# Performance work log

Measured on AMD Instinct MI355X. Metric: run time of the kernel, lower is better.

Reference implementation:

```python
import jax, jax.numpy as jnp
import numpy as np

D_K = 64
NEG_INF = -1.0e9


def setup_inputs() -> dict:
    key = jax.random.key(0)
    kq, kk, kv, km = jax.random.split(key, 4)
    B, H, S, D = 4, 16, 2048, D_K
    q = jax.random.normal(kq, (B, H, S, D), dtype=jnp.float32)
    k = jax.random.normal(kk, (B, H, S, D), dtype=jnp.float32)
    v = jax.random.normal(kv, (B, H, S, D), dtype=jnp.float32)
    attn_mask = jax.random.randint(km, (B, H, S, S), 0, 2).astype(jnp.bool_)
    return {"q": q, "k": k, "v": v, "attn_mask": attn_mask}


def reference(q, k, v, attn_mask):
    # scores: [B,H,S,S] = q @ k^T / sqrt(d_k)
    scale = 1.0 / jnp.sqrt(jnp.float32(D_K)).astype(q.dtype)
    attn_score = jnp.einsum("bhqd,bhkd->bhqk", q, k) * scale
    attn_score = jnp.where(attn_mask, jnp.asarray(NEG_INF, attn_score.dtype), attn_score)
    attn_weights = jax.nn.softmax(attn_score, axis=-1)
    # dropout p=0.0 -> identity (deterministic reference)
    output = jnp.einsum("bhqk,bhkd->bhqd", attn_weights, v)
    return (output, attn_weights)
```

## Files before the change

### kernel.cpp

```cpp
#include <hip/hip_runtime.h>
#include <hip/hip_bf16.h>

#define S_LEN 2048
#define DK    64
#define NT64  32
#define O_ELEMS (4 * 16 * 2048 * 64)

typedef float f32x4  __attribute__((ext_vector_type(4)));
typedef short bf16x8 __attribute__((ext_vector_type(8)));

static __device__ __forceinline__ unsigned short f2bf(float f) {
  unsigned int u = __builtin_bit_cast(unsigned int, f);
  u += 0x7fffu + ((u >> 16) & 1u);
  return (unsigned short)(u >> 16);
}

static __device__ __forceinline__ void gload_lds16(const void* g, void* l) {
  __builtin_amdgcn_global_load_lds(
      (const __attribute__((address_space(1))) unsigned int*)g,
      (__attribute__((address_space(3))) unsigned int*)l, 16, 0, 0);
}

__global__ __launch_bounds__(256) void cvt_k_kernel(
    const float* __restrict__ k, unsigned short* __restrict__ k_hi) {
  int i = blockIdx.x * 256 + threadIdx.x;
  float4 v = ((const float4*)k)[i];
  ushort4 h;
  h.x = f2bf(v.x); h.y = f2bf(v.y); h.z = f2bf(v.z); h.w = f2bf(v.w);
  ((ushort4*)k_hi)[i] = h;
}

__global__ __launch_bounds__(256) void transpose_v_kernel(
    const float* __restrict__ v, unsigned short* __restrict__ v_t) {
  __shared__ float tile[64][65];
  const int b  = blockIdx.x;
  const int bh = b >> 5;
  const int j0 = (b & 31) << 6;
  const int t  = threadIdx.x;
  #pragma unroll
  for (int i = 0; i < 4; ++i) {
    int flat = i * 256 + t;
    int jl   = flat >> 4;
    int f4   = flat & 15;
    float4 x = *(const float4*)(v + ((size_t)bh * S_LEN + j0 + jl) * DK + f4 * 4);
    tile[jl][f4 * 4 + 0] = x.x;
    tile[jl][f4 * 4 + 1] = x.y;
    tile[jl][f4 * 4 + 2] = x.z;
    tile[jl][f4 * 4 + 3] = x.w;
  }
  __syncthreads();
  #pragma unroll
  for (int i = 0; i < 4; ++i) {
    int flat = i * 256 + t;
    int d    = flat >> 4;
    int jg   = (flat & 15) << 2;
    ushort4 o;
    o.x = f2bf(tile[jg + 0][d]);
    o.y = f2bf(tile[jg + 1][d]);
    o.z = f2bf(tile[jg + 2][d]);
    o.w = f2bf(tile[jg + 3][d]);
    *(ushort4*)(v_t + ((size_t)bh * DK + d) * S_LEN + j0 + jg) = o;
  }
}

__global__ __launch_bounds__(256, 2) void attn_main(
    const float* __restrict__ q,
    const int* __restrict__ mask,
    const unsigned short* __restrict__ k_hi,
    const unsigned short* __restrict__ v_t,
    float* __restrict__ out_o,
    float* __restrict__ out_w) {
  const int blk = blockIdx.x;
  const int id  = ((blk & 7) << 8) | (blk >> 3);
  const int bh  = id >> 5;
  const int q0  = (id & 31) << 6;

  const int tid = threadIdx.x;
  const int w   = tid >> 6;
  const int ln  = tid & 63;
  const int l15 = ln & 15;
  const int lq  = ln >> 4;

  __shared__ __align__(16) unsigned short kh_s[2][64][64];
  __shared__ __align__(16) unsigned short vt_s[2][64][64];
  __shared__ __align__(16) int            m_lds[2][64][64];
  __shared__ __align__(16) unsigned short p_lds[4][16][64];

  const int r8  = ln >> 3, c8 = ln & 7;
  const int swz = c8 ^ r8;
  const size_t kst = ((size_t)bh * S_LEN + 16 * w + r8) * DK + ((size_t)swz << 3);
  const size_t vst = ((size_t)bh * DK + 16 * w + r8) * S_LEN + ((size_t)swz << 3);
  const int* mbase = mask + ((size_t)bh * S_LEN + q0 + 16 * w + (ln >> 4)) * S_LEN
                          + ((ln & 15) << 2);

  auto stage_K = [&](int t, int b) {
    gload_lds16(k_hi + kst + (size_t)t * (64 * DK),          &kh_s[b][16 * w][0]);
    gload_lds16(k_hi + kst + (size_t)t * (64 * DK) + 8 * DK, &kh_s[b][16 * w + 8][0]);
  };
  auto stage_V = [&](int t, int b) {
    gload_lds16(v_t + vst + (size_t)t * 64,             &vt_s[b][16 * w][0]);
    gload_lds16(v_t + vst + (size_t)t * 64 + 8 * S_LEN, &vt_s[b][16 * w + 8][0]);
  };
  auto stage_M = [&](int t, int b) {
    #pragma unroll
    for (int u = 0; u < 4; ++u) {
      gload_lds16(mbase + (size_t)(4 * u) * S_LEN + t * 64,
                  &m_lds[b][16 * w + 4 * u][0]);
    }
  };

  const float* qp = q + ((size_t)bh * S_LEN + q0 + (w << 4) + l15) * DK + (lq << 3);
  const float4 qa0 = *(const float4*)(qp);
  const float4 qb0 = *(const float4*)(qp + 4);
  const float4 qa1 = *(const float4*)(qp + 32);
  const float4 qb1 = *(const float4*)(qp + 36);

  stage_K(0, 0);
  stage_M(0, 0);

  bf16x8 qh[2];
  {
    const float sc = 0.125f * 1.4426950408889634f;
    float vv0[8] = {qa0.x, qa0.y, qa0.z, qa0.w, qb0.x, qb0.y, qb0.z, qb0.w};
    float vv1[8] = {qa1.x, qa1.y, qa1.z, qa1.w, qb1.x, qb1.y, qb1.z, qb1.w};
    #pragma unroll
    for (int i = 0; i < 8; ++i) {
      qh[0][i] = (short)f2bf(vv0[i] * sc);
      qh[1][i] = (short)f2bf(vv1[i] * sc);
    }
  }

  const size_t rowb = (size_t)bh * S_LEN + q0 + (w << 4) + (lq << 2);
  const size_t mofs = rowb * S_LEN + l15;
  const size_t oofs = rowb * DK + l15;
  const int rowblk = (w << 4) + (lq << 2);

  auto qk_tile = [&](const unsigned short* kbase, f32x4 (&acc)[4]) {
    #pragma unroll
    for (int s = 0; s < 4; ++s) {
      #pragma unroll
      for (int c = 0; c < 2; ++c) {
        const int off = (s * 16 + l15) * 64 + ((((c << 2) | lq) ^ (l15 & 7)) << 3);
        const bf16x8 bhf = *(const bf16x8*)(kbase + off);
        acc[s] = __builtin_amdgcn_mfma_f32_16x16x32_bf16(qh[c], bhf, acc[s], 0, 0, 0);
      }
    }
  };

  float sums[4] = {0.f, 0.f, 0.f, 0.f};
  unsigned mwv[4][4];
  #pragma unroll
  for (int r = 0; r < 4; ++r)
    #pragma unroll
    for (int wo = 0; wo < 4; ++wo) mwv[r][wo] = 0u;

#define PA_BODY(T, BUF, WMID)                                                \
  {                                                                          \
    asm volatile("s_waitcnt vmcnt(4)" ::: "memory");                         \
    __builtin_amdgcn_s_barrier();                                            \
    __builtin_amdgcn_sched_barrier(0);                                       \
    if ((T) + 1 < NT64) { stage_K((T) + 1, (BUF) ^ 1);                       \
                          stage_M((T) + 1, (BUF) ^ 1); }                     \
    f32x4 acc[4];                                                            \
    acc[0] = f32x4{0.f, 0.f, 0.f, 0.f}; acc[1] = f32x4{0.f, 0.f, 0.f, 0.f};  \
    acc[2] = f32x4{0.f, 0.f, 0.f, 0.f}; acc[3] = f32x4{0.f, 0.f, 0.f, 0.f};  \
    qk_tile(&kh_s[BUF][0][0], acc);                                          \
    asm volatile("s_waitcnt vmcnt(" #WMID ")" ::: "memory");                 \
    __builtin_amdgcn_sched_barrier(0);                                       \
    _Pragma("unroll") for (int r = 0; r < 4; ++r) {                          \
      _Pragma("unroll") for (int s = 0; s < 4; ++s) {                        \
        const int mv = m_lds[BUF][rowblk + r][s * 16 + l15];                 \
        mwv[r][(T) >> 3] |= (unsigned)(mv != 0) << (4 * ((T) & 7) + s);      \
        sums[r] += mv ? 0.f : __builtin_amdgcn_exp2f(acc[s][r]);             \
      }                                                                      \
    }                                                                        \
  }

  PA_BODY(0, 0, 6);
  for (int tt = 0; tt < 15; ++tt) {
    PA_BODY(2 * tt + 1, 1, 6);
    PA_BODY(2 * tt + 2, 0, 6);
  }
  PA_BODY(31, 1, 0);

  #pragma unroll
  for (int r = 0; r < 4; ++r) {
    float x = sums[r];
    x += __shfl_xor(x, 1, 64);
    x += __shfl_xor(x, 2, 64);
    x += __shfl_xor(x, 4, 64);
    x += __shfl_xor(x, 8, 64);
    sums[r] = 1.0f / x;
  }

  f32x4 oacc[4];
  #pragma unroll
  for (int s = 0; s < 4; ++s) oacc[s] = f32x4{0.f, 0.f, 0.f, 0.f};

  stage_K(0, 0);
  stage_V(0, 0);

#define PB_BODY(T, BUF, WAITN)                                               \
  {                                                                          \
    asm volatile("s_waitcnt vmcnt(" #WAITN ")" ::: "memory");                \
    __builtin_amdgcn_s_barrier();                                            \
    __builtin_amdgcn_sched_barrier(0);                                       \
    if ((T) + 1 < NT64) { stage_K((T) + 1, (BUF) ^ 1);                       \
                          stage_V((T) + 1, (BUF) ^ 1); }                     \
    f32x4 acc[4];                                                            \
    acc[0] = f32x4{0.f, 0.f, 0.f, 0.f}; acc[1] = f32x4{0.f, 0.f, 0.f, 0.f};  \
    acc[2] = f32x4{0.f, 0.f, 0.f, 0.f}; acc[3] = f32x4{0.f, 0.f, 0.f, 0.f};  \
    qk_tile(&kh_s[BUF][0][0], acc);                                          \
    const int sh0 = 4 * ((T) & 7);                                           \
    float* wbase = out_w + mofs + (size_t)(T) * 64;                          \
    _Pragma("unroll") for (int r = 0; r < 4; ++r) {                          \
      const unsigned mword = mwv[r][(T) >> 3];                               \
      const int row = (lq << 2) + r;                                         \
      _Pragma("unroll") for (int s = 0; s < 4; ++s) {                        \
        const int m = (int)((mword >> (sh0 + s)) & 1u);                      \
        const float e = m ? 0.f : __builtin_amdgcn_exp2f(acc[s][r]);         \
        const float wn = e * sums[r];                                        \
        wbase[(size_t)r * S_LEN + s * 16] = wn;                              \
        const int chunk = ((s << 1) | (l15 >> 3)) ^ (row & 7);               \
        p_lds[w][row][(chunk << 3) | (l15 & 7)] = f2bf(wn);                  \
      }                                                                      \
    }                                                                        \
    __builtin_amdgcn_wave_barrier();                                         \
    _Pragma("unroll") for (int c = 0; c < 2; ++c) {                          \
      const bf16x8 pa = *(const bf16x8*)                                     \
          &p_lds[w][l15][((((c << 2) | lq)) ^ (l15 & 7)) << 3];              \
      _Pragma("unroll") for (int s = 0; s < 4; ++s) {                        \
        const int off = (s * 16 + l15) * 64 +                                \
                        ((((c << 2) | lq) ^ (l15 & 7)) << 3);                \
        const bf16x8 vb = *(const bf16x8*)(&vt_s[BUF][0][0] + off);          \
        oacc[s] = __builtin_amdgcn_mfma_f32_16x16x32_bf16(pa, vb, oacc[s],   \
                                                          0, 0, 0);          \
      }                                                                      \
    }                                                                        \
    __builtin_amdgcn_wave_barrier();                                         \
  }

  PB_BODY(0, 0, 0);
  for (int tt = 0; tt < 15; ++tt) {
    PB_BODY(2 * tt + 1, 1, 16);
    PB_BODY(2 * tt + 2, 0, 16);
  }
  PB_BODY(31, 1, 16);

  #pragma unroll
  for (int s = 0; s < 4; ++s) {
    #pragma unroll
    for (int r = 0; r < 4; ++r) {
      out_o[oofs + (size_t)r * DK + s * 16] = oacc[s][r];
    }
  }
#undef PA_BODY
#undef PB_BODY
}

extern "C" void kernel_launch(void* const* d_in, const int* in_sizes, int n_in,
                              void* d_out, int out_size, void* d_ws, size_t ws_size,
                              hipStream_t stream) {
  (void)in_sizes; (void)n_in; (void)out_size; (void)ws_size;
  const float* q = (const float*)d_in[0];
  const float* k = (const float*)d_in[1];
  const float* v = (const float*)d_in[2];
  const int* mask = (const int*)d_in[3];

  float* out_o = (float*)d_out;
  float* out_w = out_o + (size_t)O_ELEMS;

  unsigned short* k_hi = (unsigned short*)d_ws;
  unsigned short* v_t  = k_hi + (size_t)O_ELEMS;

  cvt_k_kernel<<<8192, 256, 0, stream>>>(k, k_hi);
  transpose_v_kernel<<<2048, 256, 0, stream>>>(v, v_t);
  attn_main<<<2048, 256, 0, stream>>>(q, mask, k_hi, v_t, out_o, out_w);
}
```

Before: 665.4 us.

## Split attention into separate score-sum and PV kernels with packed mask bits

Splits the fused two-pass attention kernel into a first kernel that computes softmax denominators and packs the mask into bitwords, and a second kernel that recomputes scores, writes weights and does the PV product. Mask loads move from async LDS staging to direct register loads, which drops the large mask LDS buffer so each kernel can target higher occupancy (launch bounds 4). The cost is an extra launch and writing then reading the packed bits and sums through global memory.

```diff
diff --git a/kernel.cpp b/kernel.cpp
--- a/kernel.cpp
+++ b/kernel.cpp
@@ -63,9 +63,127 @@
   }
 }
 
-__global__ __launch_bounds__(256, 2) void attn_main(
+__global__ __launch_bounds__(256, 4) void score_sums(
     const float* __restrict__ q,
     const int* __restrict__ mask,
+    const unsigned short* __restrict__ k_hi,
+    unsigned int* __restrict__ bits,
+    float* __restrict__ sums_out) {
+  const int blk = blockIdx.x;
+  const int id  = ((blk & 7) << 8) | (blk >> 3);
+  const int bh  = id >> 5;
+  const int q0  = (id & 31) << 6;
+  const int tid = threadIdx.x;
+  const int w   = tid >> 6;
+  const int ln  = tid & 63;
+  const int l15 = ln & 15;
+  const int lq  = ln >> 4;
+
+  __shared__ __align__(16) unsigned short kh_s[2][64][64];
+
+  const int r8  = ln >> 3, c8 = ln & 7;
+  const int swz = c8 ^ r8;
+  const size_t kst = ((size_t)bh * S_LEN + 16 * w + r8) * DK + ((size_t)swz << 3);
+  auto stage_K = [&](int t, int b) {
+    gload_lds16(k_hi + kst + (size_t)t * (64 * DK),          &kh_s[b][16 * w][0]);
+    gload_lds16(k_hi + kst + (size_t)t * (64 * DK) + 8 * DK, &kh_s[b][16 * w + 8][0]);
+  };
+
+  const float* qp = q + ((size_t)bh * S_LEN + q0 + (w << 4) + l15) * DK + (lq << 3);
+  const float4 qa0 = *(const float4*)(qp);
+  const float4 qb0 = *(const float4*)(qp + 4);
+  const float4 qa1 = *(const float4*)(qp + 32);
+  const float4 qb1 = *(const float4*)(qp + 36);
+
+  const size_t rowb = (size_t)bh * S_LEN + q0 + (w << 4) + (lq << 2);
+  const int* mptr = mask + rowb * S_LEN + l15;
+
+  bf16x8 qh[2];
+  {
+    const float sc = 0.125f * 1.4426950408889634f;
+    float vv0[8] = {qa0.x, qa0.y, qa0.z, qa0.w, qb0.x, qb0.y, qb0.z, qb0.w};
+    float vv1[8] = {qa1.x, qa1.y, qa1.z, qa1.w, qb1.x, qb1.y, qb1.z, qb1.w};
+    #pragma unroll
+    for (int i = 0; i < 8; ++i) {
+      qh[0][i] = (short)f2bf(vv0[i] * sc);
+      qh[1][i] = (short)f2bf(vv1[i] * sc);
+    }
+  }
+
+  auto qk_tile = [&](const unsigned short* kbase, f32x4 (&acc)[4]) {
+    #pragma unroll
+    for (int s = 0; s < 4; ++s) {
+      #pragma unroll
+      for (int c = 0; c < 2; ++c) {
+        const int off = (s * 16 + l15) * 64 + ((((c << 2) | lq) ^ (l15 & 7)) << 3);
+        const bf16x8 bhf = *(const bf16x8*)(kbase + off);
+        acc[s] = __builtin_amdgcn_mfma_f32_16x16x32_bf16(qh[c], bhf, acc[s], 0, 0, 0);
+      }
+    }
+  };
+
+  unsigned mA[16], mB[16];
+  float sums[4] = {0.f, 0.f, 0.f, 0.f};
+  unsigned mwv[4][4];
+  #pragma unroll
+  for (int r = 0; r < 4; ++r)
+    #pragma unroll
+    for (int wo = 0; wo < 4; ++wo) mwv[r][wo] = 0u;
+
+#define LOAD_M(T, M)                                                         \
+  _Pragma("unroll") for (int r = 0; r < 4; ++r)                              \
+    _Pragma("unroll") for (int s = 0; s < 4; ++s)                            \
+      M[r * 4 + s] = (unsigned)mptr[(size_t)r * S_LEN + (T) * 64 + s * 16];
+
+  stage_K(0, 0);
+  LOAD_M(0, mA)
+  __syncthreads();
+
+#define SA_BODY(T, BUF, MC, MN)                                              \
+  {                                                                          \
+    if ((T) + 1 < NT64) { stage_K((T) + 1, (BUF) ^ 1); LOAD_M((T) + 1, MN) } \
+    f32x4 acc[4];                                                            \
+    acc[0] = f32x4{0.f, 0.f, 0.f, 0.f}; acc[1] = f32x4{0.f, 0.f, 0.f, 0.f};  \
+    acc[2] = f32x4{0.f, 0.f, 0.f, 0.f}; acc[3] = f32x4{0.f, 0.f, 0.f, 0.f};  \
+    qk_tile(&kh_s[BUF][0][0], acc);                                          \
+    _Pragma("unroll") for (int r = 0; r < 4; ++r) {                          \
+      _Pragma("unroll") for (int s = 0; s < 4; ++s) {                        \
+        const unsigned mv = MC[r * 4 + s];                                   \
+        mwv[r][(T) >> 3] |= (unsigned)(mv != 0) << (4 * ((T) & 7) + s);      \
+        sums[r] += mv ? 0.f : __builtin_amdgcn_exp2f(acc[s][r]);             \
+      }                                                                      \
+    }                                                                        \
+    __syncthreads();                                                         \
+  }
+
+  SA_BODY(0, 0, mA, mB)
+  for (int tt = 0; tt < 15; ++tt) {
+    SA_BODY(2 * tt + 1, 1, mB, mA)
+    SA_BODY(2 * tt + 2, 0, mA, mB)
+  }
+  SA_BODY(31, 1, mB, mA)
+
+  #pragma unroll
+  for (int r = 0; r < 4; ++r) {
+    float x = sums[r];
+    x += __shfl_xor(x, 1, 64);
+    x += __shfl_xor(x, 2, 64);
+    x += __shfl_xor(x, 4, 64);
+    x += __shfl_xor(x, 8, 64);
+    if (l15 == 0) sums_out[id * 64 + (w << 4) + (lq << 2) + r] = 1.0f / x;
+  }
+  unsigned int* bb = bits + ((size_t)id * 256 + tid) * 16;
+  #pragma unroll
+  for (int r = 0; r < 4; ++r)
+    *(uint4*)(bb + 4 * r) = make_uint4(mwv[r][0], mwv[r][1], mwv[r][2], mwv[r][3]);
+#undef SA_BODY
+#undef LOAD_M
+}
+
+__global__ __launch_bounds__(256, 4) void attn_pv(
+    const float* __restrict__ q,
+    const unsigned int* __restrict__ bits,
+    const float* __restrict__ sums_in,
     const unsigned short* __restrict__ k_hi,
     const unsigned short* __restrict__ v_t,
     float* __restrict__ out_o,
@@ -74,7 +192,6 @@
   const int id  = ((blk & 7) << 8) | (blk >> 3);
   const int bh  = id >> 5;
   const int q0  = (id & 31) << 6;
-
   const int tid = threadIdx.x;
   const int w   = tid >> 6;
   const int ln  = tid & 63;
@@ -83,15 +200,12 @@
 
   __shared__ __align__(16) unsigned short kh_s[2][64][64];
   __shared__ __align__(16) unsigned short vt_s[2][64][64];
-  __shared__ __align__(16) int            m_lds[2][64][64];
   __shared__ __align__(16) unsigned short p_lds[4][16][64];
 
   const int r8  = ln >> 3, c8 = ln & 7;
   const int swz = c8 ^ r8;
   const size_t kst = ((size_t)bh * S_LEN + 16 * w + r8) * DK + ((size_t)swz << 3);
   const size_t vst = ((size_t)bh * DK + 16 * w + r8) * S_LEN + ((size_t)swz << 3);
-  const int* mbase = mask + ((size_t)bh * S_LEN + q0 + 16 * w + (ln >> 4)) * S_LEN
-                          + ((ln & 15) << 2);
 
   auto stage_K = [&](int t, int b) {
     gload_lds16(k_hi + kst + (size_t)t * (64 * DK),          &kh_s[b][16 * w][0]);
@@ -100,13 +214,6 @@
   auto stage_V = [&](int t, int b) {
     gload_lds16(v_t + vst + (size_t)t * 64,             &vt_s[b][16 * w][0]);
     gload_lds16(v_t + vst + (size_t)t * 64 + 8 * S_LEN, &vt_s[b][16 * w + 8][0]);
-  };
-  auto stage_M = [&](int t, int b) {
-    #pragma unroll
-    for (int u = 0; u < 4; ++u) {
-      gload_lds16(mbase + (size_t)(4 * u) * S_LEN + t * 64,
-                  &m_lds[b][16 * w + 4 * u][0]);
-    }
   };
 
   const float* qp = q + ((size_t)bh * S_LEN + q0 + (w << 4) + l15) * DK + (lq << 3);
@@ -114,9 +221,12 @@
   const float4 qb0 = *(const float4*)(qp + 4);
   const float4 qa1 = *(const float4*)(qp + 32);
   const float4 qb1 = *(const float4*)(qp + 36);
-
-  stage_K(0, 0);
-  stage_M(0, 0);
+  const uint4* bq = (const uint4*)(bits + ((size_t)id * 256 + tid) * 16);
+  uint4 mq[4];
+  #pragma unroll
+  for (int r = 0; r < 4; ++r) mq[r] = bq[r];
+  const float* sp = sums_in + id * 64 + (w << 4) + (lq << 2);
+  float sums[4] = {sp[0], sp[1], sp[2], sp[3]};
 
   bf16x8 qh[2];
   {
@@ -133,7 +243,6 @@
   const size_t rowb = (size_t)bh * S_LEN + q0 + (w << 4) + (lq << 2);
   const size_t mofs = rowb * S_LEN + l15;
   const size_t oofs = rowb * DK + l15;
-  const int rowblk = (w << 4) + (lq << 2);
 
   auto qk_tile = [&](const unsigned short* kbase, f32x4 (&acc)[4]) {
     #pragma unroll
@@ -147,52 +256,6 @@
     }
   };
 
-  float sums[4] = {0.f, 0.f, 0.f, 0.f};
-  unsigned mwv[4][4];
-  #pragma unroll
-  for (int r = 0; r < 4; ++r)
-    #pragma unroll
-    for (int wo = 0; wo < 4; ++wo) mwv[r][wo] = 0u;
-
-#define PA_BODY(T, BUF, WMID)                                                \
-  {                                                                          \
-    asm volatile("s_waitcnt vmcnt(4)" ::: "memory");                         \
-    __builtin_amdgcn_s_barrier();                                            \
-    __builtin_amdgcn_sched_barrier(0);                                       \
-    if ((T) + 1 < NT64) { stage_K((T) + 1, (BUF) ^ 1);                       \
-                          stage_M((T) + 1, (BUF) ^ 1); }                     \
-    f32x4 acc[4];                                                            \
-    acc[0] = f32x4{0.f, 0.f, 0.f, 0.f}; acc[1] = f32x4{0.f, 0.f, 0.f, 0.f};  \
-    acc[2] = f32x4{0.f, 0.f, 0.f, 0.f}; acc[3] = f32x4{0.f, 0.f, 0.f, 0.f};  \
-    qk_tile(&kh_s[BUF][0][0], acc);                                          \
-    asm volatile("s_waitcnt vmcnt(" #WMID ")" ::: "memory");                 \
-    __builtin_amdgcn_sched_barrier(0);                                       \
-    _Pragma("unroll") for (int r = 0; r < 4; ++r) {                          \
-      _Pragma("unroll") for (int s = 0; s < 4; ++s) {                        \
-        const int mv = m_lds[BUF][rowblk + r][s * 16 + l15];                 \
-        mwv[r][(T) >> 3] |= (unsigned)(mv != 0) << (4 * ((T) & 7) + s);      \
-        sums[r] += mv ? 0.f : __builtin_amdgcn_exp2f(acc[s][r]);             \
-      }                                                                      \
-    }                                                                        \
-  }
-
-  PA_BODY(0, 0, 6);
-  for (int tt = 0; tt < 15; ++tt) {
-    PA_BODY(2 * tt + 1, 1, 6);
-    PA_BODY(2 * tt + 2, 0, 6);
-  }
-  PA_BODY(31, 1, 0);
-
-  #pragma unroll
-  for (int r = 0; r < 4; ++r) {
-    float x = sums[r];
-    x += __shfl_xor(x, 1, 64);
-    x += __shfl_xor(x, 2, 64);
-    x += __shfl_xor(x, 4, 64);
-    x += __shfl_xor(x, 8, 64);
-    sums[r] = 1.0f / x;
-  }
-
   f32x4 oacc[4];
   #pragma unroll
   for (int s = 0; s < 4; ++s) oacc[s] = f32x4{0.f, 0.f, 0.f, 0.f};
@@ -207,14 +270,17 @@
     __builtin_amdgcn_sched_barrier(0);                                       \
     if ((T) + 1 < NT64) { stage_K((T) + 1, (BUF) ^ 1);                       \
                           stage_V((T) + 1, (BUF) ^ 1); }                     \
+    __builtin_amdgcn_sched_barrier(0);      \
     f32x4 acc[4];                                                            \
     acc[0] = f32x4{0.f, 0.f, 0.f, 0.f}; acc[1] = f32x4{0.f, 0.f, 0.f, 0.f};  \
     acc[2] = f32x4{0.f, 0.f, 0.f, 0.f}; acc[3] = f32x4{0.f, 0.f, 0.f, 0.f};  \
     qk_tile(&kh_s[BUF][0][0], acc);                                          \
+    const int wsel = (T) >> 3;                                               \
     const int sh0 = 4 * ((T) & 7);                                           \
     float* wbase = out_w + mofs + (size_t)(T) * 64;                          \
     _Pragma("unroll") for (int r = 0; r < 4; ++r) {                          \
-      const unsigned mword = mwv[r][(T) >> 3];                               \
+      const unsigned mword = wsel == 0 ? mq[r].x : wsel == 1 ? mq[r].y       \
+                           : wsel == 2 ? mq[r].z : mq[r].w;                  \
       const int row = (lq << 2) + r;                                         \
       _Pragma("unroll") for (int s = 0; s < 4; ++s) {                        \
         const int m = (int)((mword >> (sh0 + s)) & 1u);                      \
@@ -240,12 +306,12 @@
     __builtin_amdgcn_wave_barrier();                                         \
   }
 
-  PB_BODY(0, 0, 0);
+  PB_BODY(0, 0, 0)
   for (int tt = 0; tt < 15; ++tt) {
-    PB_BODY(2 * tt + 1, 1, 16);
-    PB_BODY(2 * tt + 2, 0, 16);
-  }
-  PB_BODY(31, 1, 16);
+    PB_BODY(2 * tt + 1, 1, 16)
+    PB_BODY(2 * tt + 2, 0, 16)
+  }
+  PB_BODY(31, 1, 16)
 
   #pragma unroll
   for (int s = 0; s < 4; ++s) {
@@ -254,7 +320,6 @@
       out_o[oofs + (size_t)r * DK + s * 16] = oacc[s][r];
     }
   }
-#undef PA_BODY
 #undef PB_BODY
 }
 
@@ -272,8 +337,11 @@
 
   unsigned short* k_hi = (unsigned short*)d_ws;
   unsigned short* v_t  = k_hi + (size_t)O_ELEMS;
+  unsigned int*   bits = (unsigned int*)(v_t + (size_t)O_ELEMS);
+  float*          sums = (float*)(bits + (size_t)2048 * 256 * 16);
 
   cvt_k_kernel<<<8192, 256, 0, stream>>>(k, k_hi);
   transpose_v_kernel<<<2048, 256, 0, stream>>>(v, v_t);
-  attn_main<<<2048, 256, 0, stream>>>(q, mask, k_hi, v_t, out_o, out_w);
-}
+  score_sums<<<2048, 256, 0, stream>>>(q, mask, k_hi, bits, sums);
+  attn_pv<<<2048, 256, 0, stream>>>(q, bits, sums, k_hi, v_t, out_o, out_w);
+}
```

Result: faster. 589.9 us (-11.3%).
